# Optimization experiments

Measured on AMD Instinct MI355X. Metric: run time of the kernel, lower is better.

The kernel has to match this reference:

```python
import jax, jax.numpy as jnp
import numpy as np

B, S, D = 16, 16, 4096
H, KV, HD = 32, 8, 128
MAX_B, MAX_S = 16, 4096
START = 4080


def setup_inputs() -> dict:
    key = jax.random.key(0)
    ks = jax.random.split(key, 10)
    sc = 0.02
    # RoPE angles for positions [START, START+S)
    inv_freq = 1.0 / (10000.0 ** (np.arange(0, HD, 2, dtype=np.float32) / HD))  # [HD/2]
    pos = np.arange(START, START + S, dtype=np.float32)
    ang = np.outer(pos, inv_freq)  # [S, HD/2]
    return {
        'x': jax.random.normal(ks[0], (B, S, D), jnp.float32),
        'k': jax.random.normal(ks[1], (B, S, D), jnp.float32),
        'v': jax.random.normal(ks[2], (B, S, D), jnp.float32),
        'wq': jax.random.normal(ks[3], (D, H * HD), jnp.float32) * sc,
        'wk': jax.random.normal(ks[4], (D, KV * HD), jnp.float32) * sc,
        'wv': jax.random.normal(ks[5], (D, KV * HD), jnp.float32) * sc,
        'wo': jax.random.normal(ks[6], (H * HD, D), jnp.float32) * sc,
        'cache_k': jax.random.normal(ks[7], (MAX_B, MAX_S, KV, HD), jnp.float32),
        'cache_v': jax.random.normal(ks[8], (MAX_B, MAX_S, KV, HD), jnp.float32),
        'freqs_cos': jnp.asarray(np.cos(ang)),
        'freqs_sin': jnp.asarray(np.sin(ang)),
        'start_pos': START,
    }


def _rope(t, cos, sin):
    # t: [B,S,nh,HD]; interleaved complex pairs (even=real, odd=imag)
    t2 = t.reshape(*t.shape[:-1], HD // 2, 2)
    x0, x1 = t2[..., 0], t2[..., 1]
    c = cos[None, :, None, :]
    s = sin[None, :, None, :]
    r0 = x0 * c - x1 * s
    r1 = x0 * s + x1 * c
    return jnp.stack([r0, r1], axis=-1).reshape(t.shape)


def reference(x, k, v, wq, wk, wv, wo, cache_k, cache_v, freqs_cos, freqs_sin, start_pos):
    rep = H // KV
    xq = (x @ wq).reshape(B, S, H, HD)
    xk = (k @ wk).reshape(B, S, KV, HD)
    xv = (v @ wv).reshape(B, S, KV, HD)
    xq = _rope(xq, freqs_cos, freqs_sin)
    xk = _rope(xk, freqs_cos, freqs_sin)
    # KV-cache append (start_pos is a static Python int)
    cache_k = jax.lax.dynamic_update_slice(cache_k, xk, (0, start_pos, 0, 0))
    cache_v = jax.lax.dynamic_update_slice(cache_v, xv, (0, start_pos, 0, 0))
    T = start_pos + S
    keys = cache_k[:B, :T]    # [B,T,KV,HD]
    values = cache_v[:B, :T]  # [B,T,KV,HD]
    # GQA without materializing repeat_kv: q head h = g*rep + r
    q = xq.reshape(B, S, KV, rep, HD)
    scores = jnp.einsum('bsgrd,btgd->bgrst', q, keys) / jnp.sqrt(jnp.float32(HD))
    attn = jax.nn.softmax(scores.astype(jnp.float32), axis=-1).astype(q.dtype)
    out = jnp.einsum('bgrst,btgd->bsgrd', attn, values).reshape(B, S, H * HD)
    return out @ wo
```

## Files before the change

### kernel.cpp

```cpp
#include <hip/hip_runtime.h>

typedef __attribute__((ext_vector_type(8))) short bf8_t;
typedef __attribute__((ext_vector_type(4))) short s4_t;
typedef __attribute__((ext_vector_type(4))) float f4_t;
typedef __attribute__((ext_vector_type(4))) unsigned u4_t;

#define DEV static __device__ __forceinline__

DEV short f2bf(float f) {
  union { float f; unsigned u; } x; x.f = f;
  unsigned r = x.u + 0x7FFFu + ((x.u >> 16) & 1u);
  return (short)(r >> 16);
}
DEV float bf2f(short h) {
  union { unsigned u; float f; } x; x.u = ((unsigned)(unsigned short)h) << 16;
  return x.f;
}
DEV unsigned pk2(float a, float b) {
  return (unsigned)(unsigned short)f2bf(a) |
         ((unsigned)(unsigned short)f2bf(b) << 16);
}
DEV f4_t mfma16(bf8_t a, bf8_t b, f4_t c) {
  return __builtin_amdgcn_mfma_f32_16x16x32_bf16(a, b, c, 0, 0, 0);
}
DEV f4_t zf4() { f4_t v = {0.f, 0.f, 0.f, 0.f}; return v; }

DEV void cvt8(const f4_t& f0, const f4_t& f1, bf8_t& hv, bf8_t& lv) {
#pragma unroll
  for (int i = 0; i < 4; i++) {
    short h = f2bf(f0[i]); hv[i] = h; lv[i] = f2bf(f0[i] - bf2f(h));
  }
#pragma unroll
  for (int i = 0; i < 4; i++) {
    short h = f2bf(f1[i]); hv[4 + i] = h; lv[4 + i] = f2bf(f1[i] - bf2f(h));
  }
}

__global__ __launch_bounds__(256, 4)
void qkv_kernel(const float* __restrict__ x, const float* __restrict__ kin,
                const float* __restrict__ vin, const float* __restrict__ wq,
                const float* __restrict__ wk, const float* __restrict__ wv,
                float* __restrict__ part)
{
  __shared__ short Bh[2][64][40], Bl[2][64][40];

  int bid = blockIdx.x;
  int sw = (bid & 7) * 192 + (bid >> 3);
  int ks = sw / 384;
  int r  = sw % 384;

  int lin, N, cbase;
  const float* A; const float* W;
  if (r < 256)      { lin = r;       A = x;   W = wq; N = 4096; cbase = 0; }
  else if (r < 320) { lin = r - 256; A = kin; W = wk; N = 1024; cbase = 4096; }
  else              { lin = r - 320; A = vin; W = wv; N = 1024; cbase = 5120; }
  int m0 = (lin & 3) * 64;
  int n0 = (lin >> 2) * 64;
  int k0 = ks * 1024;

  int tid = threadIdx.x, w = tid >> 6, l = tid & 63;
  f4_t acc[4];
#pragma unroll
  for (int i = 0; i < 4; i++) acc[i] = zf4();

  int bn = tid & 63;
  int bch = (tid >> 6) ^ ((tid >> 3) & 3);
  int bk = bch * 8;
  const float* wptr = W + n0 + bn;

  const float* afrag = A + (m0 + w * 16 + (l & 15)) * 4096 + k0 + (l >> 4) * 8;

  f4_t a0 = *(const f4_t*)afrag;
  f4_t a1 = *(const f4_t*)(afrag + 4);
  float br[8];
#pragma unroll
  for (int j = 0; j < 8; j++) br[j] = wptr[(size_t)(k0 + bk + j) * N];

  for (int it = 0; it < 32; ++it) {
    int cur = it & 1;
    {
      f4_t f0, f1;
#pragma unroll
      for (int j = 0; j < 4; j++) { f0[j] = br[j]; f1[j] = br[4 + j]; }
      bf8_t hv, lv; cvt8(f0, f1, hv, lv);
      *(bf8_t*)&Bh[cur][bn][bk] = hv;
      *(bf8_t*)&Bl[cur][bn][bk] = lv;
    }
    f4_t a0c = a0, a1c = a1;
    if (it + 1 < 32) {
      a0 = *(const f4_t*)(afrag + (it + 1) * 32);
      a1 = *(const f4_t*)(afrag + (it + 1) * 32 + 4);
#pragma unroll
      for (int j = 0; j < 8; j++)
        br[j] = wptr[(size_t)(k0 + (it + 1) * 32 + bk + j) * N];
    }
    __syncthreads();
    bf8_t ah, al; cvt8(a0c, a1c, ah, al);
    __builtin_amdgcn_s_setprio(1);
#pragma unroll
    for (int nt = 0; nt < 4; ++nt) {
      bf8_t bh = *(const bf8_t*)&Bh[cur][nt * 16 + (l & 15)][(l >> 4) * 8];
      bf8_t bl = *(const bf8_t*)&Bl[cur][nt * 16 + (l & 15)][(l >> 4) * 8];
      acc[nt] = mfma16(ah, bh, acc[nt]);
      acc[nt] = mfma16(ah, bl, acc[nt]);
      acc[nt] = mfma16(al, bh, acc[nt]);
    }
    __builtin_amdgcn_s_setprio(0);
  }

  float* po = part + ((size_t)ks * 256 + m0) * 6144 + cbase + n0;
  int cl = l & 15, gq = l >> 4;
#pragma unroll
  for (int nt = 0; nt < 4; ++nt)
#pragma unroll
    for (int i = 0; i < 4; i++)
      po[(w * 16 + gq * 4 + i) * 6144 + nt * 16 + cl] = acc[nt][i];
}

__global__ __launch_bounds__(256)
void reduce_rope(const float* __restrict__ part,
                 const float* __restrict__ fcos, const float* __restrict__ fsin,
                 short* __restrict__ qh, short* __restrict__ ql,
                 float* __restrict__ kf, float* __restrict__ vf)
{
  int gid = blockIdx.x * 256 + threadIdx.x;
  int row = gid / 768;
  int c8  = (gid - row * 768) * 8;
  const float* p = part + (size_t)row * 6144 + c8;
  float v[8];
#pragma unroll
  for (int j = 0; j < 8; j++) v[j] = p[j];
#pragma unroll
  for (int ksp = 1; ksp < 4; ksp++) {
    const float* q = p + (size_t)ksp * 256 * 6144;
#pragma unroll
    for (int j = 0; j < 8; j++) v[j] += q[j];
  }
  int s = row & 15, bb = row >> 4;
  if (c8 < 4096) {
    int h = c8 >> 7, d = c8 & 127;
    f4_t c  = *(const f4_t*)(fcos + s * 64 + (d >> 1));
    f4_t sn = *(const f4_t*)(fsin + s * 64 + (d >> 1));
    bf8_t hv, lv;
#pragma unroll
    for (int pr = 0; pr < 4; pr++) {
      float x0 = v[2 * pr], x1 = v[2 * pr + 1];
      float r0 = (x0 * c[pr] - x1 * sn[pr]) * 0.08838834764831845f;
      float r1 = (x0 * sn[pr] + x1 * c[pr]) * 0.08838834764831845f;
      short h0 = f2bf(r0); hv[2 * pr] = h0; lv[2 * pr] = f2bf(r0 - bf2f(h0));
      short h1 = f2bf(r1); hv[2 * pr + 1] = h1; lv[2 * pr + 1] = f2bf(r1 - bf2f(h1));
    }
    int idx = ((bb * 8 + (h >> 2)) * 64 + (h & 3) * 16 + s) * 128 + d;
    *(bf8_t*)(qh + idx) = hv;
    *(bf8_t*)(ql + idx) = lv;
  } else if (c8 < 5120) {
    int cc = c8 - 4096; int h = cc >> 7, d = cc & 127;
    f4_t c  = *(const f4_t*)(fcos + s * 64 + (d >> 1));
    f4_t sn = *(const f4_t*)(fsin + s * 64 + (d >> 1));
    f4_t o0, o1;
#pragma unroll
    for (int pr = 0; pr < 2; pr++) {
      float x0 = v[2 * pr], x1 = v[2 * pr + 1];
      o0[2 * pr]     = x0 * c[pr] - x1 * sn[pr];
      o0[2 * pr + 1] = x0 * sn[pr] + x1 * c[pr];
    }
#pragma unroll
    for (int pr = 2; pr < 4; pr++) {
      float x0 = v[2 * pr], x1 = v[2 * pr + 1];
      o1[2 * (pr - 2)]     = x0 * c[pr] - x1 * sn[pr];
      o1[2 * (pr - 2) + 1] = x0 * sn[pr] + x1 * c[pr];
    }
    size_t idx = (((size_t)bb * 16 + s) * 8 + h) * 128 + d;
    *(f4_t*)(kf + idx) = o0;
    *(f4_t*)(kf + idx + 4) = o1;
  } else {
    int cc = c8 - 5120; int h = cc >> 7, d = cc & 127;
    size_t idx = (((size_t)bb * 16 + s) * 8 + h) * 128 + d;
    f4_t o0, o1;
#pragma unroll
    for (int j = 0; j < 4; j++) { o0[j] = v[j]; o1[j] = v[4 + j]; }
    *(f4_t*)(vf + idx) = o0;
    *(f4_t*)(vf + idx + 4) = o1;
  }
}

__global__ __launch_bounds__(256, 3)
void attn_kernel(const float* __restrict__ ck, const float* __restrict__ cv,
                 const short* __restrict__ qhp, const short* __restrict__ qlp,
                 const float* __restrict__ kfp, const float* __restrict__ vfp,
                 const int* __restrict__ startp,
                 float* __restrict__ Op, float* __restrict__ mp,
                 float* __restrict__ lp)
{
  __shared__ short Kh[32][136];
  __shared__ short Vt[128][40];
  __shared__ short Ps[4][16][40];

  int bid = blockIdx.x;
  int bg = bid >> 3, sp = bid & 7;
  int b = bg >> 3, g = bg & 7;
  int tid = threadIdx.x, w = tid >> 6, l = tid & 63;
  int start = *startp;

  bf8_t qfh[4], qfl[4];
  {
    int qoff = (bg * 64 + w * 16 + (l & 15)) * 128 + (l >> 4) * 8;
#pragma unroll
    for (int kt = 0; kt < 4; ++kt) {
      qfh[kt] = *(const bf8_t*)(qhp + qoff + kt * 32);
      qfl[kt] = *(const bf8_t*)(qlp + qoff + kt * 32);
    }
  }
  f4_t of[8];
#pragma unroll
  for (int i = 0; i < 8; i++) of[i] = zf4();
  float mrun[4], lrun[4];
#pragma unroll
  for (int i = 0; i < 4; i++) { mrun[i] = -1e30f; lrun[i] = 0.f; }

  int st_t = tid >> 3;
  int d0   = (tid & 7) * 16;
  int rr   = (tid >> 3) & 7;
  int oo   = tid >> 6;

  f4_t kr[4], vr[4];

  auto ISSUE = [&](int tile) {
    int t = sp * 512 + tile * 32 + st_t;
    size_t o_st = (((size_t)b * 4096 + t) * 8 + g) * 128;
    size_t o_fr = (((size_t)b * 16 + (size_t)(t - start)) * 8 + g) * 128;
    const float* kp_ = (t < start) ? (ck + o_st) : (kfp + o_fr);
    const float* vp_ = (t < start) ? (cv + o_st) : (vfp + o_fr);
#pragma unroll
    for (int j = 0; j < 4; j++) kr[j] = *(const f4_t*)(kp_ + d0 + 4 * j);
#pragma unroll
    for (int j = 0; j < 4; j++) vr[j] = *(const f4_t*)(vp_ + d0 + 4 * j);
  };

  auto WRITE = [&]() {
    unsigned kp[8];
#pragma unroll
    for (int p = 0; p < 8; p++)
      kp[p] = pk2(kr[p >> 1][(p & 1) * 2], kr[p >> 1][(p & 1) * 2 + 1]);
    u4_t kw0 = {kp[0], kp[1], kp[2], kp[3]};
    u4_t kw1 = {kp[4], kp[5], kp[6], kp[7]};
    *(u4_t*)&Kh[st_t][d0] = kw0;
    *(u4_t*)&Kh[st_t][d0 + 8] = kw1;

    unsigned vp[8];
#pragma unroll
    for (int p = 0; p < 8; p++)
      vp[p] = pk2(vr[p >> 1][(p & 1) * 2], vr[p >> 1][(p & 1) * 2 + 1]);
#pragma unroll
    for (int kk = 1; kk < 8; kk <<= 1) {
      unsigned nv[8];
#pragma unroll
      for (int i = 0; i < 8; i++) {
        unsigned ex = __shfl_xor(vp[i ^ kk], kk * 8);
        bool sw = (((i & kk) != 0) != ((rr & kk) != 0));
        nv[i] = sw ? ex : vp[i];
      }
#pragma unroll
      for (int i = 0; i < 8; i++) vp[i] = nv[i];
    }
    u4_t ra, rb;
#pragma unroll
    for (int i = 0; i < 4; i++) {
      ra[i] = (vp[2 * i] & 0xffffu) | (vp[2 * i + 1] << 16);
      rb[i] = (vp[2 * i] >> 16) | (vp[2 * i + 1] & 0xffff0000u);
    }
    *(u4_t*)&Vt[d0 + 2 * rr][oo * 8] = ra;
    *(u4_t*)&Vt[d0 + 2 * rr + 1][oo * 8] = rb;
  };

  ISSUE(0);
  WRITE();
  __syncthreads();
  ISSUE(1);

  for (int tile = 0; tile < 16; ++tile) {
    f4_t sf[2];
#pragma unroll
    for (int i = 0; i < 2; i++) sf[i] = zf4();
    __builtin_amdgcn_s_setprio(1);
#pragma unroll
    for (int tt = 0; tt < 2; ++tt)
#pragma unroll
      for (int kt = 0; kt < 4; ++kt) {
        bf8_t kb = *(const bf8_t*)&Kh[tt * 16 + (l & 15)][kt * 32 + (l >> 4) * 8];
        sf[tt] = mfma16(qfh[kt], kb, sf[tt]);
        sf[tt] = mfma16(qfl[kt], kb, sf[tt]);
      }
    __builtin_amdgcn_s_setprio(0);

    float mt[4];
#pragma unroll
    for (int i = 0; i < 4; i++) mt[i] = fmaxf(sf[0][i], sf[1][i]);
#pragma unroll
    for (int st = 1; st < 16; st <<= 1)
#pragma unroll
      for (int i = 0; i < 4; i++) mt[i] = fmaxf(mt[i], __shfl_xor(mt[i], st));
    float sc[4];
#pragma unroll
    for (int i = 0; i < 4; i++) {
      float mn = fmaxf(mrun[i], mt[i]);
      sc[i] = __expf(mrun[i] - mn);
      mrun[i] = mn;
    }
    float rs[4] = {0.f, 0.f, 0.f, 0.f};
#pragma unroll
    for (int tt = 0; tt < 2; ++tt)
#pragma unroll
      for (int i = 0; i < 4; i++) {
        float pexp = __expf(sf[tt][i] - mrun[i]);
        rs[i] += pexp;
        Ps[w][(l >> 4) * 4 + i][tt * 16 + (l & 15)] = f2bf(pexp);
      }
#pragma unroll
    for (int st = 1; st < 16; st <<= 1)
#pragma unroll
      for (int i = 0; i < 4; i++) rs[i] += __shfl_xor(rs[i], st);
#pragma unroll
    for (int i = 0; i < 4; i++) lrun[i] = lrun[i] * sc[i] + rs[i];
#pragma unroll
    for (int dt = 0; dt < 8; ++dt)
#pragma unroll
      for (int i = 0; i < 4; i++) of[dt][i] *= sc[i];

    __builtin_amdgcn_s_setprio(1);
    {
      bf8_t pa = *(const bf8_t*)&Ps[w][l & 15][(l >> 4) * 8];
#pragma unroll
      for (int dt = 0; dt < 8; ++dt) {
        bf8_t vfr = *(const bf8_t*)&Vt[dt * 16 + (l & 15)][(l >> 4) * 8];
        of[dt] = mfma16(pa, vfr, of[dt]);
      }
    }
    __builtin_amdgcn_s_setprio(0);

    if (tile < 15) {
      __syncthreads();
      WRITE();
      __syncthreads();
      if (tile < 14) ISSUE(tile + 2);
    }
  }

  size_t obase = ((size_t)(bg * 8 + sp) * 64 + w * 16) * 128;
#pragma unroll
  for (int dt = 0; dt < 8; ++dt)
#pragma unroll
    for (int i = 0; i < 4; i++)
      Op[obase + ((l >> 4) * 4 + i) * 128 + dt * 16 + (l & 15)] = of[dt][i];
  if ((l & 15) == 0) {
    int rbase = (bg * 8 + sp) * 64 + w * 16 + (l >> 4) * 4;
#pragma unroll
    for (int i = 0; i < 4; i++) { mp[rbase + i] = mrun[i]; lp[rbase + i] = lrun[i]; }
  }
}

__global__ __launch_bounds__(256)
void merge_kernel(const float* __restrict__ Op, const float* __restrict__ mp,
                  const float* __restrict__ lp, short* __restrict__ attnb)
{
  int bg = blockIdx.x;
  int tid = threadIdx.x;
  int row = tid >> 2, dc = (tid & 3) * 32;
  int b = bg >> 3, g = bg & 7;
  int r = row >> 4, s = row & 15;
  float mm[8], ww[8];
  float M = -1e30f;
#pragma unroll
  for (int spp = 0; spp < 8; ++spp) {
    mm[spp] = mp[(bg * 8 + spp) * 64 + row];
    M = fmaxf(M, mm[spp]);
  }
  float denom = 0.f;
#pragma unroll
  for (int spp = 0; spp < 8; ++spp) {
    ww[spp] = __expf(mm[spp] - M);
    denom += lp[(bg * 8 + spp) * 64 + row] * ww[spp];
  }
  float inv = 1.0f / denom;
  int ob = (b * 16 + s) * 4096 + (g * 4 + r) * 128 + dc;
#pragma unroll
  for (int j = 0; j < 8; j++) {
    f4_t a = zf4();
#pragma unroll
    for (int spp = 0; spp < 8; ++spp) {
      f4_t o = *(const f4_t*)(Op + ((size_t)(bg * 8 + spp) * 64 + row) * 128 + dc + j * 4);
#pragma unroll
      for (int i = 0; i < 4; i++) a[i] += ww[spp] * o[i];
    }
    s4_t o4;
#pragma unroll
    for (int i = 0; i < 4; i++) o4[i] = f2bf(a[i] * inv);
    *(s4_t*)(attnb + ob + j * 4) = o4;
  }
}

__global__ __launch_bounds__(256, 4)
void wo_kernel(const short* __restrict__ attnb, const float* __restrict__ wo,
               float* __restrict__ wpart)
{
  __shared__ short Bs[2][64][40];

  int bid = blockIdx.x;
  int sw = (bid & 7) * 128 + (bid >> 3);
  int ks = sw >> 8, r = sw & 255;
  int m0 = (r & 3) * 64, n0 = (r >> 2) * 64, k0 = ks * 1024;

  int tid = threadIdx.x, w = tid >> 6, l = tid & 63;
  f4_t acc[4];
#pragma unroll
  for (int i = 0; i < 4; i++) acc[i] = zf4();

  int bn = tid & 63;
  int bch = (tid >> 6) ^ ((tid >> 3) & 3);
  int bk = bch * 8;
  const float* wptr = wo + n0 + bn;
  const short* afrag = attnb + (m0 + w * 16 + (l & 15)) * 4096 + k0 + (l >> 4) * 8;

  bf8_t areg = *(const bf8_t*)afrag;
  float br[8];
#pragma unroll
  for (int j = 0; j < 8; j++) br[j] = wptr[(size_t)(k0 + bk + j) * 4096];

  for (int it = 0; it < 32; ++it) {
    int cur = it & 1;
    {
      bf8_t hv;
#pragma unroll
      for (int j = 0; j < 8; j++) hv[j] = f2bf(br[j]);
      *(bf8_t*)&Bs[cur][bn][bk] = hv;
    }
    bf8_t ac = areg;
    if (it + 1 < 32) {
      areg = *(const bf8_t*)(afrag + (it + 1) * 32);
#pragma unroll
      for (int j = 0; j < 8; j++)
        br[j] = wptr[(size_t)(k0 + (it + 1) * 32 + bk + j) * 4096];
    }
    __syncthreads();
    __builtin_amdgcn_s_setprio(1);
#pragma unroll
    for (int nt = 0; nt < 4; ++nt) {
      bf8_t bb_ = *(const bf8_t*)&Bs[cur][nt * 16 + (l & 15)][(l >> 4) * 8];
      acc[nt] = mfma16(ac, bb_, acc[nt]);
    }
    __builtin_amdgcn_s_setprio(0);
  }

  float* po = wpart + ((size_t)ks * 256 + m0) * 4096 + n0;
  int cl = l & 15, gq = l >> 4;
#pragma unroll
  for (int nt = 0; nt < 4; ++nt)
#pragma unroll
    for (int i = 0; i < 4; i++)
      po[(w * 16 + gq * 4 + i) * 4096 + nt * 16 + cl] = acc[nt][i];
}

__global__ __launch_bounds__(256)
void reduce_out(const float* __restrict__ wpart, float* __restrict__ out)
{
  int gid = blockIdx.x * 256 + threadIdx.x;
  size_t idx4 = (size_t)gid * 4;
  f4_t s = *(const f4_t*)(wpart + idx4);
#pragma unroll
  for (int ksp = 1; ksp < 4; ksp++) {
    f4_t t = *(const f4_t*)(wpart + (size_t)ksp * 1048576 + idx4);
#pragma unroll
    for (int i = 0; i < 4; i++) s[i] += t[i];
  }
  *(f4_t*)(out + idx4) = s;
}

extern "C" void kernel_launch(void* const* d_in, const int* in_sizes, int n_in,
                              void* d_out, int out_size, void* d_ws, size_t ws_size,
                              hipStream_t stream)
{
  const float* x  = (const float*)d_in[0];
  const float* k  = (const float*)d_in[1];
  const float* v  = (const float*)d_in[2];
  const float* wq = (const float*)d_in[3];
  const float* wk = (const float*)d_in[4];
  const float* wv = (const float*)d_in[5];
  const float* wo = (const float*)d_in[6];
  const float* ck = (const float*)d_in[7];
  const float* cv = (const float*)d_in[8];
  const float* fc = (const float*)d_in[9];
  const float* fs = (const float*)d_in[10];
  const int*   spv = (const int*)d_in[11];
  float* out = (float*)d_out;

  char* p = (char*)d_ws;
  float* S = (float*)p; p += (size_t)34 * 1024 * 1024;
  float* qpart = S;
  float* Oppp  = S;
  float* wpart = S;
  short* qh = (short*)p; p += (size_t)128 * 64 * 128 * 2;
  short* ql = (short*)p; p += (size_t)128 * 64 * 128 * 2;
  float* kf = (float*)p; p += (size_t)256 * 8 * 128 * 4;
  float* vf = (float*)p; p += (size_t)256 * 8 * 128 * 4;
  short* attnb = (short*)p; p += (size_t)256 * 4096 * 2;
  float* mp = (float*)p; p += (size_t)1024 * 64 * 4;
  float* lp = (float*)p; p += (size_t)1024 * 64 * 4;

  hipLaunchKernelGGL(qkv_kernel, dim3(1536), dim3(256), 0, stream,
                     x, k, v, wq, wk, wv, qpart);
  hipLaunchKernelGGL(reduce_rope, dim3(768), dim3(256), 0, stream,
                     qpart, fc, fs, qh, ql, kf, vf);
  hipLaunchKernelGGL(attn_kernel, dim3(1024), dim3(256), 0, stream,
                     ck, cv, qh, ql, kf, vf, spv, Oppp, mp, lp);
  hipLaunchKernelGGL(merge_kernel, dim3(128), dim3(256), 0, stream,
                     Oppp, mp, lp, attnb);
  hipLaunchKernelGGL(wo_kernel, dim3(1024), dim3(256), 0, stream,
                     attnb, wo, wpart);
  hipLaunchKernelGGL(reduce_out, dim3(1024), dim3(256), 0, stream,
                     wpart, out);
}
```

Before: 290.0 us.

## Deepen global prefetch to two stages and drop Q low-part split precision

```diff
diff --git a/kernel.cpp b/kernel.cpp
--- a/kernel.cpp
+++ b/kernel.cpp
@@ -6,6 +6,21 @@
 typedef __attribute__((ext_vector_type(4))) unsigned u4_t;
 
 #define DEV static __device__ __forceinline__
+
+#define LDS_FENCE_BARRIER()                                   \
+  do {                                                        \
+    asm volatile("s_waitcnt lgkmcnt(0)" ::: "memory");        \
+    __builtin_amdgcn_sched_barrier(0);                        \
+    __builtin_amdgcn_s_barrier();                             \
+    __builtin_amdgcn_sched_barrier(0);                        \
+  } while (0)
+
+#define PLAIN_BARRIER()                                       \
+  do {                                                        \
+    __builtin_amdgcn_sched_barrier(0);                        \
+    __builtin_amdgcn_s_barrier();                             \
+    __builtin_amdgcn_sched_barrier(0);                        \
+  } while (0)
 
 DEV short f2bf(float f) {
   union { float f; unsigned u; } x; x.f = f;
@@ -72,40 +87,48 @@
 
   f4_t a0 = *(const f4_t*)afrag;
   f4_t a1 = *(const f4_t*)(afrag + 4);
-  float br[8];
-#pragma unroll
-  for (int j = 0; j < 8; j++) br[j] = wptr[(size_t)(k0 + bk + j) * N];
-
-  for (int it = 0; it < 32; ++it) {
-    int cur = it & 1;
+  float brA[8], brB[8];
+#pragma unroll
+  for (int j = 0; j < 8; j++) brA[j] = wptr[(size_t)(k0 + bk + j) * N];
+#pragma unroll
+  for (int j = 0; j < 8; j++) brB[j] = wptr[(size_t)(k0 + 32 + bk + j) * N];
+
+  auto body = [&](int it, float (&br)[8], int buf) {
     {
       f4_t f0, f1;
 #pragma unroll
       for (int j = 0; j < 4; j++) { f0[j] = br[j]; f1[j] = br[4 + j]; }
       bf8_t hv, lv; cvt8(f0, f1, hv, lv);
-      *(bf8_t*)&Bh[cur][bn][bk] = hv;
-      *(bf8_t*)&Bl[cur][bn][bk] = lv;
+      *(bf8_t*)&Bh[buf][bn][bk] = hv;
+      *(bf8_t*)&Bl[buf][bn][bk] = lv;
     }
     f4_t a0c = a0, a1c = a1;
     if (it + 1 < 32) {
       a0 = *(const f4_t*)(afrag + (it + 1) * 32);
       a1 = *(const f4_t*)(afrag + (it + 1) * 32 + 4);
+    }
+    if (it + 2 < 32) {
 #pragma unroll
       for (int j = 0; j < 8; j++)
-        br[j] = wptr[(size_t)(k0 + (it + 1) * 32 + bk + j) * N];
-    }
-    __syncthreads();
+        br[j] = wptr[(size_t)(k0 + (it + 2) * 32 + bk + j) * N];
+    }
+    LDS_FENCE_BARRIER();
     bf8_t ah, al; cvt8(a0c, a1c, ah, al);
     __builtin_amdgcn_s_setprio(1);
 #pragma unroll
     for (int nt = 0; nt < 4; ++nt) {
-      bf8_t bh = *(const bf8_t*)&Bh[cur][nt * 16 + (l & 15)][(l >> 4) * 8];
-      bf8_t bl = *(const bf8_t*)&Bl[cur][nt * 16 + (l & 15)][(l >> 4) * 8];
+      bf8_t bh = *(const bf8_t*)&Bh[buf][nt * 16 + (l & 15)][(l >> 4) * 8];
+      bf8_t bl = *(const bf8_t*)&Bl[buf][nt * 16 + (l & 15)][(l >> 4) * 8];
       acc[nt] = mfma16(ah, bh, acc[nt]);
       acc[nt] = mfma16(ah, bl, acc[nt]);
       acc[nt] = mfma16(al, bh, acc[nt]);
     }
     __builtin_amdgcn_s_setprio(0);
+  };
+
+  for (int p = 0; p < 16; ++p) {
+    body(2 * p,     brA, 0);
+    body(2 * p + 1, brB, 1);
   }
 
   float* po = part + ((size_t)ks * 256 + m0) * 6144 + cbase + n0;
@@ -120,7 +143,7 @@
 __global__ __launch_bounds__(256)
 void reduce_rope(const float* __restrict__ part,
                  const float* __restrict__ fcos, const float* __restrict__ fsin,
-                 short* __restrict__ qh, short* __restrict__ ql,
+                 short* __restrict__ qh,
                  float* __restrict__ kf, float* __restrict__ vf)
 {
   int gid = blockIdx.x * 256 + threadIdx.x;
@@ -141,18 +164,17 @@
     int h = c8 >> 7, d = c8 & 127;
     f4_t c  = *(const f4_t*)(fcos + s * 64 + (d >> 1));
     f4_t sn = *(const f4_t*)(fsin + s * 64 + (d >> 1));
-    bf8_t hv, lv;
+    bf8_t hv;
 #pragma unroll
     for (int pr = 0; pr < 4; pr++) {
       float x0 = v[2 * pr], x1 = v[2 * pr + 1];
       float r0 = (x0 * c[pr] - x1 * sn[pr]) * 0.08838834764831845f;
       float r1 = (x0 * sn[pr] + x1 * c[pr]) * 0.08838834764831845f;
-      short h0 = f2bf(r0); hv[2 * pr] = h0; lv[2 * pr] = f2bf(r0 - bf2f(h0));
-      short h1 = f2bf(r1); hv[2 * pr + 1] = h1; lv[2 * pr + 1] = f2bf(r1 - bf2f(h1));
+      hv[2 * pr]     = f2bf(r0);
+      hv[2 * pr + 1] = f2bf(r1);
     }
     int idx = ((bb * 8 + (h >> 2)) * 64 + (h & 3) * 16 + s) * 128 + d;
     *(bf8_t*)(qh + idx) = hv;
-    *(bf8_t*)(ql + idx) = lv;
   } else if (c8 < 5120) {
     int cc = c8 - 4096; int h = cc >> 7, d = cc & 127;
     f4_t c  = *(const f4_t*)(fcos + s * 64 + (d >> 1));
@@ -186,7 +208,7 @@
 
 __global__ __launch_bounds__(256, 3)
 void attn_kernel(const float* __restrict__ ck, const float* __restrict__ cv,
-                 const short* __restrict__ qhp, const short* __restrict__ qlp,
+                 const short* __restrict__ qhp,
                  const float* __restrict__ kfp, const float* __restrict__ vfp,
                  const int* __restrict__ startp,
                  float* __restrict__ Op, float* __restrict__ mp,
@@ -202,14 +224,12 @@
   int tid = threadIdx.x, w = tid >> 6, l = tid & 63;
   int start = *startp;
 
-  bf8_t qfh[4], qfl[4];
+  bf8_t qfh[4];
   {
     int qoff = (bg * 64 + w * 16 + (l & 15)) * 128 + (l >> 4) * 8;
 #pragma unroll
-    for (int kt = 0; kt < 4; ++kt) {
+    for (int kt = 0; kt < 4; ++kt)
       qfh[kt] = *(const bf8_t*)(qhp + qoff + kt * 32);
-      qfl[kt] = *(const bf8_t*)(qlp + qoff + kt * 32);
-    }
   }
   f4_t of[8];
 #pragma unroll
@@ -223,9 +243,7 @@
   int rr   = (tid >> 3) & 7;
   int oo   = tid >> 6;
 
-  f4_t kr[4], vr[4];
-
-  auto ISSUE = [&](int tile) {
+  auto ISSUE = [&](int tile, f4_t (&kr)[4], f4_t (&vr)[4]) {
     int t = sp * 512 + tile * 32 + st_t;
     size_t o_st = (((size_t)b * 4096 + t) * 8 + g) * 128;
     size_t o_fr = (((size_t)b * 16 + (size_t)(t - start)) * 8 + g) * 128;
@@ -237,7 +255,7 @@
     for (int j = 0; j < 4; j++) vr[j] = *(const f4_t*)(vp_ + d0 + 4 * j);
   };
 
-  auto WRITE = [&]() {
+  auto WRITE = [&](f4_t (&kr)[4], f4_t (&vr)[4]) {
     unsigned kp[8];
 #pragma unroll
     for (int p = 0; p < 8; p++)
@@ -257,8 +275,8 @@
 #pragma unroll
       for (int i = 0; i < 8; i++) {
         unsigned ex = __shfl_xor(vp[i ^ kk], kk * 8);
-        bool sw = (((i & kk) != 0) != ((rr & kk) != 0));
-        nv[i] = sw ? ex : vp[i];
+        bool swp = (((i & kk) != 0) != ((rr & kk) != 0));
+        nv[i] = swp ? ex : vp[i];
       }
 #pragma unroll
       for (int i = 0; i < 8; i++) vp[i] = nv[i];
@@ -273,12 +291,15 @@
     *(u4_t*)&Vt[d0 + 2 * rr + 1][oo * 8] = rb;
   };
 
-  ISSUE(0);
-  WRITE();
-  __syncthreads();
-  ISSUE(1);
-
-  for (int tile = 0; tile < 16; ++tile) {
+  f4_t krA[4], vrA[4], krB[4], vrB[4];
+
+  ISSUE(0, krA, vrA);
+  ISSUE(1, krB, vrB);
+  WRITE(krA, vrA);
+  ISSUE(2, krA, vrA);
+  LDS_FENCE_BARRIER();
+
+  auto STEP = [&](int t, f4_t (&krW)[4], f4_t (&vrW)[4]) {
     f4_t sf[2];
 #pragma unroll
     for (int i = 0; i < 2; i++) sf[i] = zf4();
@@ -289,7 +310,6 @@
       for (int kt = 0; kt < 4; ++kt) {
         bf8_t kb = *(const bf8_t*)&Kh[tt * 16 + (l & 15)][kt * 32 + (l >> 4) * 8];
         sf[tt] = mfma16(qfh[kt], kb, sf[tt]);
-        sf[tt] = mfma16(qfl[kt], kb, sf[tt]);
       }
     __builtin_amdgcn_s_setprio(0);
 
@@ -338,12 +358,17 @@
     }
     __builtin_amdgcn_s_setprio(0);
 
-    if (tile < 15) {
-      __syncthreads();
-      WRITE();
-      __syncthreads();
-      if (tile < 14) ISSUE(tile + 2);
-    }
+    if (t < 15) {
+      PLAIN_BARRIER();
+      WRITE(krW, vrW);
+      if (t + 3 < 16) ISSUE(t + 3, krW, vrW);
+      LDS_FENCE_BARRIER();
+    }
+  };
+
+  for (int p = 0; p < 8; ++p) {
+    STEP(2 * p,     krB, vrB);
+    STEP(2 * p + 1, krA, vrA);
   }
 
   size_t obase = ((size_t)(bg * 8 + sp) * 64 + w * 16) * 128;
@@ -422,33 +447,39 @@
   const short* afrag = attnb + (m0 + w * 16 + (l & 15)) * 4096 + k0 + (l >> 4) * 8;
 
   bf8_t areg = *(const bf8_t*)afrag;
-  float br[8];
-#pragma unroll
-  for (int j = 0; j < 8; j++) br[j] = wptr[(size_t)(k0 + bk + j) * 4096];
-
-  for (int it = 0; it < 32; ++it) {
-    int cur = it & 1;
+  float brA[8], brB[8];
+#pragma unroll
+  for (int j = 0; j < 8; j++) brA[j] = wptr[(size_t)(k0 + bk + j) * 4096];
+#pragma unroll
+  for (int j = 0; j < 8; j++) brB[j] = wptr[(size_t)(k0 + 32 + bk + j) * 4096];
+
+  auto body = [&](int it, float (&br)[8], int buf) {
     {
       bf8_t hv;
 #pragma unroll
       for (int j = 0; j < 8; j++) hv[j] = f2bf(br[j]);
-      *(bf8_t*)&Bs[cur][bn][bk] = hv;
+      *(bf8_t*)&Bs[buf][bn][bk] = hv;
     }
     bf8_t ac = areg;
-    if (it + 1 < 32) {
-      areg = *(const bf8_t*)(afrag + (it + 1) * 32);
+    if (it + 1 < 32) areg = *(const bf8_t*)(afrag + (it + 1) * 32);
+    if (it + 2 < 32) {
 #pragma unroll
       for (int j = 0; j < 8; j++)
-        br[j] = wptr[(size_t)(k0 + (it + 1) * 32 + bk + j) * 4096];
-    }
-    __syncthreads();
+        br[j] = wptr[(size_t)(k0 + (it + 2) * 32 + bk + j) * 4096];
+    }
+    LDS_FENCE_BARRIER();
     __builtin_amdgcn_s_setprio(1);
 #pragma unroll
     for (int nt = 0; nt < 4; ++nt) {
-      bf8_t bb_ = *(const bf8_t*)&Bs[cur][nt * 16 + (l & 15)][(l >> 4) * 8];
+      bf8_t bb_ = *(const bf8_t*)&Bs[buf][nt * 16 + (l & 15)][(l >> 4) * 8];
       acc[nt] = mfma16(ac, bb_, acc[nt]);
     }
     __builtin_amdgcn_s_setprio(0);
+  };
+
+  for (int p = 0; p < 16; ++p) {
+    body(2 * p,     brA, 0);
+    body(2 * p + 1, brB, 1);
   }
 
   float* po = wpart + ((size_t)ks * 256 + m0) * 4096 + n0;
@@ -499,7 +530,6 @@
   float* Oppp  = S;
   float* wpart = S;
   short* qh = (short*)p; p += (size_t)128 * 64 * 128 * 2;
-  short* ql = (short*)p; p += (size_t)128 * 64 * 128 * 2;
   float* kf = (float*)p; p += (size_t)256 * 8 * 128 * 4;
   float* vf = (float*)p; p += (size_t)256 * 8 * 128 * 4;
   short* attnb = (short*)p; p += (size_t)256 * 4096 * 2;
@@ -509,9 +539,9 @@
   hipLaunchKernelGGL(qkv_kernel, dim3(1536), dim3(256), 0, stream,
                      x, k, v, wq, wk, wv, qpart);
   hipLaunchKernelGGL(reduce_rope, dim3(768), dim3(256), 0, stream,
-                     qpart, fc, fs, qh, ql, kf, vf);
+                     qpart, fc, fs, qh, kf, vf);
   hipLaunchKernelGGL(attn_kernel, dim3(1024), dim3(256), 0, stream,
-                     ck, cv, qh, ql, kf, vf, spv, Oppp, mp, lp);
+                     ck, cv, qh, kf, vf, spv, Oppp, mp, lp);
   hipLaunchKernelGGL(merge_kernel, dim3(128), dim3(256), 0, stream,
                      Oppp, mp, lp, attnb);
   hipLaunchKernelGGL(wo_kernel, dim3(1024), dim3(256), 0, stream,
```

Measured after the change: 320.6 us. 10.5% more time.

## Drop split-bf16 precision, pre-convert inputs, remove split-K in Wo projection

Applied to the files above, without the earlier changes.

```diff
diff --git a/kernel.cpp b/kernel.cpp
--- a/kernel.cpp
+++ b/kernel.cpp
@@ -25,24 +25,32 @@
 }
 DEV f4_t zf4() { f4_t v = {0.f, 0.f, 0.f, 0.f}; return v; }
 
-DEV void cvt8(const f4_t& f0, const f4_t& f1, bf8_t& hv, bf8_t& lv) {
-#pragma unroll
-  for (int i = 0; i < 4; i++) {
-    short h = f2bf(f0[i]); hv[i] = h; lv[i] = f2bf(f0[i] - bf2f(h));
-  }
-#pragma unroll
-  for (int i = 0; i < 4; i++) {
-    short h = f2bf(f1[i]); hv[4 + i] = h; lv[4 + i] = f2bf(f1[i] - bf2f(h));
-  }
+__global__ __launch_bounds__(256)
+void prep_inputs(const float* __restrict__ x, const float* __restrict__ k,
+                 const float* __restrict__ v, short* __restrict__ xb,
+                 short* __restrict__ kb, short* __restrict__ vb)
+{
+  int gid = blockIdx.x * 256 + threadIdx.x;
+  size_t base = (size_t)gid * 8;
+  const float* src; short* dst; size_t off;
+  if (base < 1048576)       { src = x; dst = xb; off = base; }
+  else if (base < 2097152)  { src = k; dst = kb; off = base - 1048576; }
+  else                      { src = v; dst = vb; off = base - 2097152; }
+  f4_t f0 = *(const f4_t*)(src + off);
+  f4_t f1 = *(const f4_t*)(src + off + 4);
+  bf8_t hv;
+#pragma unroll
+  for (int j = 0; j < 4; j++) { hv[j] = f2bf(f0[j]); hv[4 + j] = f2bf(f1[j]); }
+  *(bf8_t*)(dst + off) = hv;
 }
 
 __global__ __launch_bounds__(256, 4)
-void qkv_kernel(const float* __restrict__ x, const float* __restrict__ kin,
-                const float* __restrict__ vin, const float* __restrict__ wq,
+void qkv_kernel(const short* __restrict__ xb, const short* __restrict__ kb,
+                const short* __restrict__ vb, const float* __restrict__ wq,
                 const float* __restrict__ wk, const float* __restrict__ wv,
                 float* __restrict__ part)
 {
-  __shared__ short Bh[2][64][40], Bl[2][64][40];
+  __shared__ short Bs[2][64][40];
 
   int bid = blockIdx.x;
   int sw = (bid & 7) * 192 + (bid >> 3);
@@ -50,10 +58,10 @@
   int r  = sw % 384;
 
   int lin, N, cbase;
-  const float* A; const float* W;
-  if (r < 256)      { lin = r;       A = x;   W = wq; N = 4096; cbase = 0; }
-  else if (r < 320) { lin = r - 256; A = kin; W = wk; N = 1024; cbase = 4096; }
-  else              { lin = r - 320; A = vin; W = wv; N = 1024; cbase = 5120; }
+  const short* A; const float* W;
+  if (r < 256)      { lin = r;       A = xb; W = wq; N = 4096; cbase = 0; }
+  else if (r < 320) { lin = r - 256; A = kb; W = wk; N = 1024; cbase = 4096; }
+  else              { lin = r - 320; A = vb; W = wv; N = 1024; cbase = 5120; }
   int m0 = (lin & 3) * 64;
   int n0 = (lin >> 2) * 64;
   int k0 = ks * 1024;
@@ -68,44 +76,42 @@
   int bk = bch * 8;
   const float* wptr = W + n0 + bn;
 
-  const float* afrag = A + (m0 + w * 16 + (l & 15)) * 4096 + k0 + (l >> 4) * 8;
-
-  f4_t a0 = *(const f4_t*)afrag;
-  f4_t a1 = *(const f4_t*)(afrag + 4);
-  float br[8];
-#pragma unroll
-  for (int j = 0; j < 8; j++) br[j] = wptr[(size_t)(k0 + bk + j) * N];
-
-  for (int it = 0; it < 32; ++it) {
-    int cur = it & 1;
+  const short* afrag = A + (m0 + w * 16 + (l & 15)) * 4096 + k0 + (l >> 4) * 8;
+
+  bf8_t areg = *(const bf8_t*)afrag;
+  float brA[8], brB[8];
+#pragma unroll
+  for (int j = 0; j < 8; j++) brA[j] = wptr[(size_t)(k0 + bk + j) * N];
+#pragma unroll
+  for (int j = 0; j < 8; j++) brB[j] = wptr[(size_t)(k0 + 32 + bk + j) * N];
+
+  auto body = [&](int it, float (&br)[8], int buf) {
     {
-      f4_t f0, f1;
-#pragma unroll
-      for (int j = 0; j < 4; j++) { f0[j] = br[j]; f1[j] = br[4 + j]; }
-      bf8_t hv, lv; cvt8(f0, f1, hv, lv);
-      *(bf8_t*)&Bh[cur][bn][bk] = hv;
-      *(bf8_t*)&Bl[cur][bn][bk] = lv;
-    }
-    f4_t a0c = a0, a1c = a1;
-    if (it + 1 < 32) {
-      a0 = *(const f4_t*)(afrag + (it + 1) * 32);
-      a1 = *(const f4_t*)(afrag + (it + 1) * 32 + 4);
+      bf8_t hv;
+#pragma unroll
+      for (int j = 0; j < 8; j++) hv[j] = f2bf(br[j]);
+      *(bf8_t*)&Bs[buf][bn][bk] = hv;
+    }
+    bf8_t ac = areg;
+    if (it + 1 < 32) areg = *(const bf8_t*)(afrag + (it + 1) * 32);
+    if (it + 2 < 32) {
 #pragma unroll
       for (int j = 0; j < 8; j++)
-        br[j] = wptr[(size_t)(k0 + (it + 1) * 32 + bk + j) * N];
+        br[j] = wptr[(size_t)(k0 + (it + 2) * 32 + bk + j) * N];
     }
     __syncthreads();
-    bf8_t ah, al; cvt8(a0c, a1c, ah, al);
     __builtin_amdgcn_s_setprio(1);
 #pragma unroll
     for (int nt = 0; nt < 4; ++nt) {
-      bf8_t bh = *(const bf8_t*)&Bh[cur][nt * 16 + (l & 15)][(l >> 4) * 8];
-      bf8_t bl = *(const bf8_t*)&Bl[cur][nt * 16 + (l & 15)][(l >> 4) * 8];
-      acc[nt] = mfma16(ah, bh, acc[nt]);
-      acc[nt] = mfma16(ah, bl, acc[nt]);
-      acc[nt] = mfma16(al, bh, acc[nt]);
+      bf8_t bh = *(const bf8_t*)&Bs[buf][nt * 16 + (l & 15)][(l >> 4) * 8];
+      acc[nt] = mfma16(ac, bh, acc[nt]);
     }
     __builtin_amdgcn_s_setprio(0);
+  };
+
+  for (int p = 0; p < 16; ++p) {
+    body(2 * p,     brA, 0);
+    body(2 * p + 1, brB, 1);
   }
 
   float* po = part + ((size_t)ks * 256 + m0) * 6144 + cbase + n0;
@@ -120,7 +126,7 @@
 __global__ __launch_bounds__(256)
 void reduce_rope(const float* __restrict__ part,
                  const float* __restrict__ fcos, const float* __restrict__ fsin,
-                 short* __restrict__ qh, short* __restrict__ ql,
+                 short* __restrict__ qh,
                  float* __restrict__ kf, float* __restrict__ vf)
 {
   int gid = blockIdx.x * 256 + threadIdx.x;
@@ -141,18 +147,17 @@
     int h = c8 >> 7, d = c8 & 127;
     f4_t c  = *(const f4_t*)(fcos + s * 64 + (d >> 1));
     f4_t sn = *(const f4_t*)(fsin + s * 64 + (d >> 1));
-    bf8_t hv, lv;
+    bf8_t hv;
 #pragma unroll
     for (int pr = 0; pr < 4; pr++) {
       float x0 = v[2 * pr], x1 = v[2 * pr + 1];
       float r0 = (x0 * c[pr] - x1 * sn[pr]) * 0.08838834764831845f;
       float r1 = (x0 * sn[pr] + x1 * c[pr]) * 0.08838834764831845f;
-      short h0 = f2bf(r0); hv[2 * pr] = h0; lv[2 * pr] = f2bf(r0 - bf2f(h0));
-      short h1 = f2bf(r1); hv[2 * pr + 1] = h1; lv[2 * pr + 1] = f2bf(r1 - bf2f(h1));
+      hv[2 * pr]     = f2bf(r0);
+      hv[2 * pr + 1] = f2bf(r1);
     }
     int idx = ((bb * 8 + (h >> 2)) * 64 + (h & 3) * 16 + s) * 128 + d;
     *(bf8_t*)(qh + idx) = hv;
-    *(bf8_t*)(ql + idx) = lv;
   } else if (c8 < 5120) {
     int cc = c8 - 4096; int h = cc >> 7, d = cc & 127;
     f4_t c  = *(const f4_t*)(fcos + s * 64 + (d >> 1));
@@ -186,7 +191,7 @@
 
 __global__ __launch_bounds__(256, 3)
 void attn_kernel(const float* __restrict__ ck, const float* __restrict__ cv,
-                 const short* __restrict__ qhp, const short* __restrict__ qlp,
+                 const short* __restrict__ qhp,
                  const float* __restrict__ kfp, const float* __restrict__ vfp,
                  const int* __restrict__ startp,
                  float* __restrict__ Op, float* __restrict__ mp,
@@ -202,14 +207,12 @@
   int tid = threadIdx.x, w = tid >> 6, l = tid & 63;
   int start = *startp;
 
-  bf8_t qfh[4], qfl[4];
+  bf8_t qfh[4];
   {
     int qoff = (bg * 64 + w * 16 + (l & 15)) * 128 + (l >> 4) * 8;
 #pragma unroll
-    for (int kt = 0; kt < 4; ++kt) {
+    for (int kt = 0; kt < 4; ++kt)
       qfh[kt] = *(const bf8_t*)(qhp + qoff + kt * 32);
-      qfl[kt] = *(const bf8_t*)(qlp + qoff + kt * 32);
-    }
   }
   f4_t of[8];
 #pragma unroll
@@ -222,6 +225,7 @@
   int d0   = (tid & 7) * 16;
   int rr   = (tid >> 3) & 7;
   int oo   = tid >> 6;
+  int vunit = ((oo ^ (tid & 7)) & 3) * 8;
 
   f4_t kr[4], vr[4];
 
@@ -257,8 +261,8 @@
 #pragma unroll
       for (int i = 0; i < 8; i++) {
         unsigned ex = __shfl_xor(vp[i ^ kk], kk * 8);
-        bool sw = (((i & kk) != 0) != ((rr & kk) != 0));
-        nv[i] = sw ? ex : vp[i];
+        bool swp = (((i & kk) != 0) != ((rr & kk) != 0));
+        nv[i] = swp ? ex : vp[i];
       }
 #pragma unroll
       for (int i = 0; i < 8; i++) vp[i] = nv[i];
@@ -269,8 +273,8 @@
       ra[i] = (vp[2 * i] & 0xffffu) | (vp[2 * i + 1] << 16);
       rb[i] = (vp[2 * i] >> 16) | (vp[2 * i + 1] & 0xffff0000u);
     }
-    *(u4_t*)&Vt[d0 + 2 * rr][oo * 8] = ra;
-    *(u4_t*)&Vt[d0 + 2 * rr + 1][oo * 8] = rb;
+    *(u4_t*)&Vt[d0 + 2 * rr][vunit] = ra;
+    *(u4_t*)&Vt[d0 + 2 * rr + 1][vunit] = rb;
   };
 
   ISSUE(0);
@@ -289,7 +293,6 @@
       for (int kt = 0; kt < 4; ++kt) {
         bf8_t kb = *(const bf8_t*)&Kh[tt * 16 + (l & 15)][kt * 32 + (l >> 4) * 8];
         sf[tt] = mfma16(qfh[kt], kb, sf[tt]);
-        sf[tt] = mfma16(qfl[kt], kb, sf[tt]);
       }
     __builtin_amdgcn_s_setprio(0);
 
@@ -332,7 +335,7 @@
       bf8_t pa = *(const bf8_t*)&Ps[w][l & 15][(l >> 4) * 8];
 #pragma unroll
       for (int dt = 0; dt < 8; ++dt) {
-        bf8_t vfr = *(const bf8_t*)&Vt[dt * 16 + (l & 15)][(l >> 4) * 8];
+        bf8_t vfr = *(const bf8_t*)&Vt[dt * 16 + (l & 15)][(((l >> 4) ^ dt) & 3) * 8];
         of[dt] = mfma16(pa, vfr, of[dt]);
       }
     }
@@ -363,9 +366,11 @@
 void merge_kernel(const float* __restrict__ Op, const float* __restrict__ mp,
                   const float* __restrict__ lp, short* __restrict__ attnb)
 {
-  int bg = blockIdx.x;
+  int bid = blockIdx.x;
+  int bg = bid >> 2, q4 = bid & 3;
   int tid = threadIdx.x;
-  int row = tid >> 2, dc = (tid & 3) * 32;
+  int row = q4 * 16 + (tid >> 4);
+  int dc = (tid & 15) * 8;
   int b = bg >> 3, g = bg & 7;
   int r = row >> 4, s = row & 15;
   float mm[8], ww[8];
@@ -382,97 +387,90 @@
     denom += lp[(bg * 8 + spp) * 64 + row] * ww[spp];
   }
   float inv = 1.0f / denom;
+  f4_t a0 = zf4(), a1 = zf4();
+#pragma unroll
+  for (int spp = 0; spp < 8; ++spp) {
+    const float* o = Op + ((size_t)(bg * 8 + spp) * 64 + row) * 128 + dc;
+    f4_t x0 = *(const f4_t*)o;
+    f4_t x1 = *(const f4_t*)(o + 4);
+#pragma unroll
+    for (int i = 0; i < 4; i++) { a0[i] += ww[spp] * x0[i]; a1[i] += ww[spp] * x1[i]; }
+  }
   int ob = (b * 16 + s) * 4096 + (g * 4 + r) * 128 + dc;
-#pragma unroll
-  for (int j = 0; j < 8; j++) {
-    f4_t a = zf4();
-#pragma unroll
-    for (int spp = 0; spp < 8; ++spp) {
-      f4_t o = *(const f4_t*)(Op + ((size_t)(bg * 8 + spp) * 64 + row) * 128 + dc + j * 4);
-#pragma unroll
-      for (int i = 0; i < 4; i++) a[i] += ww[spp] * o[i];
-    }
-    s4_t o4;
-#pragma unroll
-    for (int i = 0; i < 4; i++) o4[i] = f2bf(a[i] * inv);
-    *(s4_t*)(attnb + ob + j * 4) = o4;
-  }
-}
-
-__global__ __launch_bounds__(256, 4)
+  bf8_t o8;
+#pragma unroll
+  for (int i = 0; i < 4; i++) {
+    o8[i]     = f2bf(a0[i] * inv);
+    o8[4 + i] = f2bf(a1[i] * inv);
+  }
+  *(bf8_t*)(attnb + ob) = o8;
+}
+
+__global__ __launch_bounds__(256, 3)
 void wo_kernel(const short* __restrict__ attnb, const float* __restrict__ wo,
-               float* __restrict__ wpart)
+               float* __restrict__ out)
 {
   __shared__ short Bs[2][64][40];
 
   int bid = blockIdx.x;
-  int sw = (bid & 7) * 128 + (bid >> 3);
-  int ks = sw >> 8, r = sw & 255;
-  int m0 = (r & 3) * 64, n0 = (r >> 2) * 64, k0 = ks * 1024;
+  int lin = (bid & 7) * 64 + (bid >> 3);
+  int m0 = (lin & 7) * 32, n0 = (lin >> 3) * 64;
 
   int tid = threadIdx.x, w = tid >> 6, l = tid & 63;
-  f4_t acc[4];
-#pragma unroll
-  for (int i = 0; i < 4; i++) acc[i] = zf4();
+  f4_t acc[2];
+#pragma unroll
+  for (int i = 0; i < 2; i++) acc[i] = zf4();
 
   int bn = tid & 63;
   int bch = (tid >> 6) ^ ((tid >> 3) & 3);
   int bk = bch * 8;
   const float* wptr = wo + n0 + bn;
-  const short* afrag = attnb + (m0 + w * 16 + (l & 15)) * 4096 + k0 + (l >> 4) * 8;
+  int n32 = (w >> 1) * 32;
+  const short* afrag = attnb + (m0 + (w & 1) * 16 + (l & 15)) * 4096 + (l >> 4) * 8;
 
   bf8_t areg = *(const bf8_t*)afrag;
-  float br[8];
-#pragma unroll
-  for (int j = 0; j < 8; j++) br[j] = wptr[(size_t)(k0 + bk + j) * 4096];
-
-  for (int it = 0; it < 32; ++it) {
-    int cur = it & 1;
+  float brA[8], brB[8];
+#pragma unroll
+  for (int j = 0; j < 8; j++) brA[j] = wptr[(size_t)(bk + j) * 4096];
+#pragma unroll
+  for (int j = 0; j < 8; j++) brB[j] = wptr[(size_t)(32 + bk + j) * 4096];
+
+  auto body = [&](int it, float (&br)[8], int buf) {
     {
       bf8_t hv;
 #pragma unroll
       for (int j = 0; j < 8; j++) hv[j] = f2bf(br[j]);
-      *(bf8_t*)&Bs[cur][bn][bk] = hv;
+      *(bf8_t*)&Bs[buf][bn][bk] = hv;
     }
     bf8_t ac = areg;
-    if (it + 1 < 32) {
-      areg = *(const bf8_t*)(afrag + (it + 1) * 32);
+    if (it + 1 < 128) areg = *(const bf8_t*)(afrag + (it + 1) * 32);
+    if (it + 2 < 128) {
 #pragma unroll
       for (int j = 0; j < 8; j++)
-        br[j] = wptr[(size_t)(k0 + (it + 1) * 32 + bk + j) * 4096];
+        br[j] = wptr[(size_t)((it + 2) * 32 + bk + j) * 4096];
     }
     __syncthreads();
     __builtin_amdgcn_s_setprio(1);
 #pragma unroll
-    for (int nt = 0; nt < 4; ++nt) {
-      bf8_t bb_ = *(const bf8_t*)&Bs[cur][nt * 16 + (l & 15)][(l >> 4) * 8];
+    for (int nt = 0; nt < 2; ++nt) {
+      bf8_t bb_ = *(const bf8_t*)&Bs[buf][n32 + nt * 16 + (l & 15)][(l >> 4) * 8];
       acc[nt] = mfma16(ac, bb_, acc[nt]);
     }
     __builtin_amdgcn_s_setprio(0);
-  }
-
-  float* po = wpart + ((size_t)ks * 256 + m0) * 4096 + n0;
+  };
+
+  for (int p = 0; p < 64; ++p) {
+    body(2 * p,     brA, 0);
+    body(2 * p + 1, brB, 1);
+  }
+
   int cl = l & 15, gq = l >> 4;
 #pragma unroll
-  for (int nt = 0; nt < 4; ++nt)
+  for (int nt = 0; nt < 2; ++nt)
 #pragma unroll
     for (int i = 0; i < 4; i++)
-      po[(w * 16 + gq * 4 + i) * 4096 + nt * 16 + cl] = acc[nt][i];
-}
-
-__global__ __launch_bounds__(256)
-void reduce_out(const float* __restrict__ wpart, float* __restrict__ out)
-{
-  int gid = blockIdx.x * 256 + threadIdx.x;
-  size_t idx4 = (size_t)gid * 4;
-  f4_t s = *(const f4_t*)(wpart + idx4);
-#pragma unroll
-  for (int ksp = 1; ksp < 4; ksp++) {
-    f4_t t = *(const f4_t*)(wpart + (size_t)ksp * 1048576 + idx4);
-#pragma unroll
-    for (int i = 0; i < 4; i++) s[i] += t[i];
-  }
-  *(f4_t*)(out + idx4) = s;
+      out[(m0 + (w & 1) * 16 + gq * 4 + i) * 4096 + n0 + n32 + nt * 16 + cl] =
+          acc[nt][i];
 }
 
 extern "C" void kernel_launch(void* const* d_in, const int* in_sizes, int n_in,
@@ -494,28 +492,29 @@
   float* out = (float*)d_out;
 
   char* p = (char*)d_ws;
-  float* S = (float*)p; p += (size_t)34 * 1024 * 1024;
+  float* S = (float*)p; p += (size_t)1024 * 64 * 128 * 4;
   float* qpart = S;
-  float* Oppp  = S;
-  float* wpart = S;
+  float* Op    = S;
+  short* xb = (short*)p; p += (size_t)256 * 4096 * 2;
+  short* kb = (short*)p; p += (size_t)256 * 4096 * 2;
+  short* vb = (short*)p; p += (size_t)256 * 4096 * 2;
   short* qh = (short*)p; p += (size_t)128 * 64 * 128 * 2;
-  short* ql = (short*)p; p += (size_t)128 * 64 * 128 * 2;
   float* kf = (float*)p; p += (size_t)256 * 8 * 128 * 4;
   float* vf = (float*)p; p += (size_t)256 * 8 * 128 * 4;
   short* attnb = (short*)p; p += (size_t)256 * 4096 * 2;
   float* mp = (float*)p; p += (size_t)1024 * 64 * 4;
   float* lp = (float*)p; p += (size_t)1024 * 64 * 4;
 
+  hipLaunchKernelGGL(prep_inputs, dim3(1536), dim3(256), 0, stream,
+                     x, k, v, xb, kb, vb);
   hipLaunchKernelGGL(qkv_kernel, dim3(1536), dim3(256), 0, stream,
-                     x, k, v, wq, wk, wv, qpart);
+                     xb, kb, vb, wq, wk, wv, qpart);
   hipLaunchKernelGGL(reduce_rope, dim3(768), dim3(256), 0, stream,
-                     qpart, fc, fs, qh, ql, kf, vf);
+                     qpart, fc, fs, qh, kf, vf);
   hipLaunchKernelGGL(attn_kernel, dim3(1024), dim3(256), 0, stream,
-                     ck, cv, qh, ql, kf, vf, spv, Oppp, mp, lp);
-  hipLaunchKernelGGL(merge_kernel, dim3(128), dim3(256), 0, stream,
-                     Oppp, mp, lp, attnb);
-  hipLaunchKernelGGL(wo_kernel, dim3(1024), dim3(256), 0, stream,
-                     attnb, wo, wpart);
-  hipLaunchKernelGGL(reduce_out, dim3(1024), dim3(256), 0, stream,
-                     wpart, out);
-}
+                     ck, cv, qh, kf, vf, spv, Op, mp, lp);
+  hipLaunchKernelGGL(merge_kernel, dim3(512), dim3(256), 0, stream,
+                     Op, mp, lp, attnb);
+  hipLaunchKernelGGL(wo_kernel, dim3(512), dim3(256), 0, stream,
+                     attnb, wo, out);
+}
```

After: 288.2 us. About the same (-0.6%).
